# Optimization experiments

Hardware: AMD Instinct MI355X
Metric: run time of the kernel (lower is better)

## Reference

```python
import jax, jax.numpy as jnp
import numpy as np

D_MODEL = 1024
NUM_HEADS = 16
HEAD_DIM = D_MODEL // NUM_HEADS
CAUSAL = True


def rope_cos_sin(seq_len, dim):
    inv_freq = 1.0 / (10000.0 ** (jnp.arange(0, dim, 2, dtype=jnp.float32) / dim))
    t = jnp.arange(seq_len, dtype=jnp.float32)
    freqs = jnp.einsum('i,j->ij', t, inv_freq)          # [S, dim/2]
    emb = jnp.concatenate([freqs, freqs], axis=-1)      # [S, dim]
    return jnp.cos(emb), jnp.sin(emb)


def rotate_half(x):
    x1, x2 = jnp.split(x, 2, axis=-1)
    return jnp.concatenate([-x2, x1], axis=-1)


def setup_inputs() -> dict:
    key = jax.random.key(0)
    k1, k2, k3, k4, k5 = jax.random.split(key, 5)
    B, S = 2, 2048
    x = jax.random.normal(k1, (B, S, D_MODEL), dtype=jnp.float32)
    s = 1.0 / np.sqrt(D_MODEL)
    W_qkv = jax.random.normal(k2, (D_MODEL, 3 * D_MODEL), dtype=jnp.float32) * s
    b_qkv = jax.random.normal(k3, (3 * D_MODEL,), dtype=jnp.float32) * 0.01
    W_out = jax.random.normal(k4, (D_MODEL, D_MODEL), dtype=jnp.float32) * s
    b_out = jax.random.normal(k5, (D_MODEL,), dtype=jnp.float32) * 0.01
    return {"x": x, "W_qkv": W_qkv, "b_qkv": b_qkv, "W_out": W_out, "b_out": b_out}


def reference(x, W_qkv, b_qkv, W_out, b_out):
    B, S, _ = x.shape
    qkv = x @ W_qkv + b_qkv                              # [B, S, 3D]
    q, k, v = jnp.split(qkv, 3, axis=-1)
    # [B, H, S, hd]
    q = q.reshape(B, S, NUM_HEADS, HEAD_DIM).transpose(0, 2, 1, 3)
    k = k.reshape(B, S, NUM_HEADS, HEAD_DIM).transpose(0, 2, 1, 3)
    v = v.reshape(B, S, NUM_HEADS, HEAD_DIM).transpose(0, 2, 1, 3)
    cos, sin = rope_cos_sin(S, HEAD_DIM)                 # [S, hd]
    cos = cos[None, None]
    sin = sin[None, None]
    q = q * cos + rotate_half(q) * sin
    k = k * cos + rotate_half(k) * sin
    scores = jnp.einsum('bhqd,bhkd->bhqk', q, k) / np.sqrt(HEAD_DIM)
    if CAUSAL:
        causal_mask = jnp.triu(jnp.ones((S, S), dtype=bool), k=1)
        scores = jnp.where(causal_mask, -jnp.inf, scores)
    attn = jax.nn.softmax(scores, axis=-1)
    out = jnp.einsum('bhqk,bhkd->bhqd', attn, v)         # [B, H, S, hd]
    out = out.transpose(0, 2, 1, 3).reshape(B, S, D_MODEL)
    return out @ W_out + b_out
```

## Files before the change

### kernel.cpp

```cpp
#include <hip/hip_runtime.h>
#include <hip/hip_bf16.h>
#include <math.h>

typedef __bf16 bf16;
typedef __bf16 bf16x8 __attribute__((ext_vector_type(8)));
typedef unsigned short ushort8 __attribute__((ext_vector_type(8)));
typedef float floatx4 __attribute__((ext_vector_type(4)));

#define MFMA_BF16(a, b, c) __builtin_amdgcn_mfma_f32_16x16x32_bf16(a, b, c, 0, 0, 0)

#define Q_SCALE 0.18033688011112042f
#define NEG_INVFREQ_LOG2 0.41524101186092029f
#define INV_2PI 0.15915494309189535f

#if __has_builtin(__builtin_amdgcn_exp2f)
#define EXP2F(x) __builtin_amdgcn_exp2f(x)
#else
#define EXP2F(x) exp2f(x)
#endif

__device__ __forceinline__ void hw_sincos_rev(float rev, float* sn, float* cs) {
#if __has_builtin(__builtin_amdgcn_sinf) && __has_builtin(__builtin_amdgcn_cosf) && \
    __has_builtin(__builtin_amdgcn_fractf)
  const float f = __builtin_amdgcn_fractf(rev);
  *sn = __builtin_amdgcn_sinf(f);
  *cs = __builtin_amdgcn_cosf(f);
#else
  sincosf(rev * 6.2831853071795864f, sn, cs);
#endif
}

__device__ __forceinline__ bf16x8 cvt8(const float4 a, const float4 b) {
  bf16x8 t;
  t[0] = (bf16)a.x; t[1] = (bf16)a.y; t[2] = (bf16)a.z; t[3] = (bf16)a.w;
  t[4] = (bf16)b.x; t[5] = (bf16)b.y; t[6] = (bf16)b.z; t[7] = (bf16)b.w;
  return t;
}

__device__ __forceinline__ unsigned int pack2(float a, float b) {
#if __has_builtin(__builtin_amdgcn_cvt_pk_bf16_f32)
  return __builtin_bit_cast(unsigned int, __builtin_amdgcn_cvt_pk_bf16_f32(a, b));
#else
  unsigned short lo = __builtin_bit_cast(unsigned short, (bf16)a);
  unsigned short hi = __builtin_bit_cast(unsigned short, (bf16)b);
  return (unsigned int)lo | ((unsigned int)hi << 16);
#endif
}

__device__ __forceinline__ void gld16(const bf16* g, bf16* l) {
  __builtin_amdgcn_global_load_lds(
      (const __attribute__((address_space(1))) unsigned int*)g,
      (__attribute__((address_space(3))) unsigned int*)l, 16, 0, 0);
}

__global__ __launch_bounds__(256) void cast_x_kernel(const float* __restrict__ in,
                                                     bf16* __restrict__ out) {
  const int i = blockIdx.x * 256 + threadIdx.x;
  const float4 a = *(const float4*)&in[(size_t)i * 8];
  const float4 b = *(const float4*)&in[(size_t)i * 8 + 4];
  *(bf16x8*)&out[(size_t)i * 8] = cvt8(a, b);
}

__global__ __launch_bounds__(256) void transpose_w_kernel(
    const float* __restrict__ in, bf16* __restrict__ out, int N, int K) {
  __shared__ __align__(16) bf16 T[64][40];
  const int t = threadIdx.x;
  const int k0 = blockIdx.y * 32, n0 = blockIdx.x * 64;
  {
    const int k = t >> 3, n8 = (t & 7) * 8;
    const float* p = &in[(size_t)(k0 + k) * N + n0 + n8];
    const float4 a = *(const float4*)p;
    const float4 b = *(const float4*)(p + 4);
    const float v[8] = {a.x, a.y, a.z, a.w, b.x, b.y, b.z, b.w};
#pragma unroll
    for (int j = 0; j < 8; j++) {
      const int n = n8 + j;
      T[n][k ^ (8 * ((n >> 3) & 3))] = (bf16)v[j];
    }
  }
  __syncthreads();
  {
    const int n = t >> 2, k8 = (t & 3) * 8;
    const int kp = k8 ^ (8 * ((n >> 3) & 3));
    *(bf16x8*)&out[(size_t)(n0 + n) * K + k0 + k8] = *(const bf16x8*)&T[n][kp];
  }
}

template <int TN, int MODE>
__global__ __launch_bounds__(256) void gemm_kernel(
    const bf16* __restrict__ A, const bf16* __restrict__ Bt,
    const float* __restrict__ bias, void* __restrict__ out0,
    bf16* __restrict__ outK, bf16* __restrict__ outV, int M, int N, int K) {
  constexpr int NI = TN / 32;
  constexpr int BI = TN / 32;
  __shared__ __align__(16) bf16 As2[2][128][32];
  __shared__ __align__(16) bf16 Bs2[2][TN][32];

  const int tid = threadIdx.x, lane = tid & 63, w = tid >> 6;
  const int c = lane & 15, quad = lane >> 4;
  const int wm = w >> 1, wn = w & 1;
  const int m0 = blockIdx.y * 128, n0 = blockIdx.x * TN;
  const int srow = lane >> 2, scol = (lane & 3) * 8;

  floatx4 acc[4][NI] = {};

  for (int k0 = 0; k0 < K; k0 += 64) {
    __syncthreads();
#pragma unroll
    for (int i = 0; i < 4; i++) {
      const int seg = w * 4 + i;
      const int kh = seg >> 3, r0 = (seg & 7) * 16;
      gld16(&A[(size_t)(m0 + r0 + srow) * K + k0 + kh * 32 + scol],
            &As2[kh][r0][0]);
    }
#pragma unroll
    for (int i = 0; i < BI; i++) {
      const int seg = w * BI + i;
      const int kh = seg / (TN / 16), r0 = (seg % (TN / 16)) * 16;
      gld16(&Bt[(size_t)(n0 + r0 + srow) * K + k0 + kh * 32 + scol],
            &Bs2[kh][r0][0]);
    }
    __syncthreads();

#pragma unroll
    for (int kh = 0; kh < 2; kh++) {
      bf16x8 af[4], bfr[NI];
#pragma unroll
      for (int mi = 0; mi < 4; mi++)
        af[mi] = *(const bf16x8*)&As2[kh][wm * 64 + mi * 16 + c][quad * 8];
#pragma unroll
      for (int ni = 0; ni < NI; ni++)
        bfr[ni] = *(const bf16x8*)&Bs2[kh][wn * (TN / 2) + ni * 16 + c][quad * 8];
#pragma unroll
      for (int mi = 0; mi < 4; mi++)
#pragma unroll
        for (int ni = 0; ni < NI; ni++)
          acc[mi][ni] = MFMA_BF16(af[mi], bfr[ni], acc[mi][ni]);
    }
  }

  if (MODE == 0) {
#pragma unroll
    for (int mi = 0; mi < 4; mi++)
#pragma unroll
      for (int ni = 0; ni < NI; ni++)
#pragma unroll
        for (int r = 0; r < 4; r++) {
          const int row = m0 + wm * 64 + mi * 16 + quad * 4 + r;
          const int col = n0 + wn * (TN / 2) + ni * 16 + c;
          ((float*)out0)[(size_t)row * N + col] = acc[mi][ni][r] + bias[col];
        }
  } else {
    const int colb = n0 + wn * (TN / 2);
    const int t = colb >> 10;
    const int h = (colb & 1023) >> 6;
    bf16* dst = (t == 0) ? (bf16*)out0 : (t == 1 ? outK : outV);
    if (t == 2) {
#pragma unroll
      for (int mi = 0; mi < 4; mi++)
#pragma unroll
        for (int ni = 0; ni < NI; ni++)
#pragma unroll
          for (int r = 0; r < 4; r++) {
            const int row = m0 + wm * 64 + mi * 16 + quad * 4 + r;
            const int col = colb + ni * 16 + c;
            const int b = row >> 11, s = row & 2047;
            dst[(((size_t)b * 16 + h) * 2048 + s) * 64 + (col & 63)] =
                (bf16)(acc[mi][ni][r] + bias[col]);
          }
    } else {
      const float qs = (t == 0) ? Q_SCALE : 1.0f;
      const float invr[2] = {exp2f(-NEG_INVFREQ_LOG2 * (float)c) * INV_2PI,
                             exp2f(-NEG_INVFREQ_LOG2 * (float)(16 + c)) * INV_2PI};
#pragma unroll
      for (int mi = 0; mi < 4; mi++) {
#pragma unroll
        for (int r = 0; r < 4; r++) {
          const int row = m0 + wm * 64 + mi * 16 + quad * 4 + r;
          const int b = row >> 11, s = row & 2047;
          const size_t base = (((size_t)b * 16 + h) * 2048 + s) * 64;
#pragma unroll
          for (int ni = 0; ni < 2; ni++) {
            float sn, cs;
            hw_sincos_rev((float)s * invr[ni], &sn, &cs);
            const float v1 = acc[mi][ni][r] + bias[colb + ni * 16 + c];
            const float v2 = acc[mi][ni + 2][r] + bias[colb + (ni + 2) * 16 + c];
            const int d = ni * 16 + c;
            dst[base + d] = (bf16)((v1 * cs - v2 * sn) * qs);
            dst[base + d + 32] = (bf16)((v2 * cs + v1 * sn) * qs);
          }
        }
      }
    }
  }
}

struct AttnState {
  floatx4 o[4];
  float l;
};

__device__ __forceinline__ void attn_step(
    const bf16x8 qf[2], const bf16x8 kf[4][2], const bf16x8 vf[4][2],
    bf16 (*PsW)[72], AttnState& st, int qglob, int kbase, bool diag, int c,
    int quad) {
  floatx4 sacc[4] = {};
#pragma unroll
  for (int kg = 0; kg < 4; kg++)
#pragma unroll
    for (int dh = 0; dh < 2; dh++)
      sacc[kg] = MFMA_BF16(kf[kg][dh], qf[dh], sacc[kg]);

#pragma unroll
  for (int kg = 0; kg < 4; kg++) {
    float p[4];
#pragma unroll
    for (int r = 0; r < 4; r++) {
      float e = EXP2F(sacc[kg][r]);
      if (diag && (kbase + kg * 16 + quad * 4 + r > qglob)) e = 0.0f;
      p[r] = e;
    }
    st.l += (p[0] + p[1]) + (p[2] + p[3]);
    const uint2 u = {pack2(p[0], p[1]), pack2(p[2], p[3])};
    *(uint2*)&PsW[c][kg * 16 + quad * 4] = u;
  }

  bf16x8 pf[2];
#pragma unroll
  for (int ks = 0; ks < 2; ks++)
    pf[ks] = *(const bf16x8*)&PsW[c][ks * 32 + quad * 8];

#pragma unroll
  for (int dg = 0; dg < 4; dg++)
#pragma unroll
    for (int ks = 0; ks < 2; ks++)
      st.o[dg] = MFMA_BF16(vf[dg][ks], pf[ks], st.o[dg]);
}

__global__ __launch_bounds__(256) void attn_kernel(const bf16* __restrict__ Q,
                                                   const bf16* __restrict__ K,
                                                   const bf16* __restrict__ V,
                                                   bf16* __restrict__ Aout) {
  const int S = 2048;
  const int bh = blockIdx.y;
  const int p = blockIdx.x;
  const int tid = threadIdx.x, lane = tid & 63, wave = tid >> 6;
  const int c = lane & 15, quad = lane >> 4;

  __shared__ __align__(16) bf16 Ks2[2][64][32];
  __shared__ __align__(16) bf16 Vt[64][72];
  __shared__ __align__(16) bf16 Ps[4][16][72];

  const bf16* Qb = Q + (size_t)bh * S * 64;
  const bf16* Kb = K + (size_t)bh * S * 64;
  const bf16* Vb = V + (size_t)bh * S * 64;
  const int b = bh >> 4, h = bh & 15;

  const int qA = p, qB = 31 - p;
  const int qgA = qA * 64 + wave * 16 + c;
  const int qgB = qB * 64 + wave * 16 + c;

  bf16x8 qfA[2], qfB[2];
#pragma unroll
  for (int dh = 0; dh < 2; dh++) {
    qfA[dh] = *(const bf16x8*)&Qb[(size_t)qgA * 64 + dh * 32 + quad * 8];
    qfB[dh] = *(const bf16x8*)&Qb[(size_t)qgB * 64 + dh * 32 + quad * 8];
  }

  AttnState stA = {}, stB = {};

  const int vcc = (tid & 7) * 8;
  const int vr2 = ((tid >> 3) + 4 * (tid & 7)) & 31;
  const int ksr = lane >> 2, ksc = (lane & 3) * 8;

  for (int kt = 0; kt <= qB; kt++) {
    __syncthreads();
#pragma unroll
    for (int i = 0; i < 2; i++) {
      const int seg = wave * 2 + i;
      const int dh = seg >> 2, r0 = (seg & 3) * 16;
      gld16(&Kb[(size_t)(kt * 64 + r0 + ksr) * 64 + dh * 32 + ksc],
            &Ks2[dh][r0][0]);
    }
    {
      const bf16* vs = &Vb[(size_t)(kt * 64 + 2 * vr2) * 64 + vcc];
      const ushort8 w0 = __builtin_bit_cast(ushort8, *(const bf16x8*)vs);
      const ushort8 w1 = __builtin_bit_cast(ushort8, *(const bf16x8*)(vs + 64));
#pragma unroll
      for (int j = 0; j < 8; j++)
        *(unsigned int*)&Vt[vcc + j][2 * vr2] =
            (unsigned int)w0[j] | ((unsigned int)w1[j] << 16);
    }
    __syncthreads();

    bf16x8 kf[4][2];
#pragma unroll
    for (int kg = 0; kg < 4; kg++)
#pragma unroll
      for (int dh = 0; dh < 2; dh++)
        kf[kg][dh] = *(const bf16x8*)&Ks2[dh][kg * 16 + c][quad * 8];

    bf16x8 vf[4][2];
#pragma unroll
    for (int dg = 0; dg < 4; dg++)
#pragma unroll
      for (int ks = 0; ks < 2; ks++)
        vf[dg][ks] = *(const bf16x8*)&Vt[dg * 16 + c][ks * 32 + quad * 8];

    attn_step(qfB, kf, vf, Ps[wave], stB, qgB, kt * 64, kt == qB, c, quad);
    if (kt <= qA)
      attn_step(qfA, kf, vf, Ps[wave], stA, qgA, kt * 64, kt == qA, c, quad);
  }

  stA.l += __shfl_xor(stA.l, 16);
  stA.l += __shfl_xor(stA.l, 32);
  stB.l += __shfl_xor(stB.l, 16);
  stB.l += __shfl_xor(stB.l, 32);
  const float ivA = 1.0f / stA.l, ivB = 1.0f / stB.l;

#pragma unroll
  for (int dg = 0; dg < 4; dg++) {
    const uint2 uA = {pack2(stA.o[dg][0] * ivA, stA.o[dg][1] * ivA),
                      pack2(stA.o[dg][2] * ivA, stA.o[dg][3] * ivA)};
    const uint2 uB = {pack2(stB.o[dg][0] * ivB, stB.o[dg][1] * ivB),
                      pack2(stB.o[dg][2] * ivB, stB.o[dg][3] * ivB)};
    *(uint2*)&Aout[((size_t)b * 2048 + qgA) * 1024 + h * 64 + dg * 16 + quad * 4] = uA;
    *(uint2*)&Aout[((size_t)b * 2048 + qgB) * 1024 + h * 64 + dg * 16 + quad * 4] = uB;
  }
}

extern "C" void kernel_launch(void* const* d_in, const int* in_sizes, int n_in,
                              void* d_out, int out_size, void* d_ws,
                              size_t ws_size, hipStream_t stream) {
  const float* x = (const float*)d_in[0];
  const float* W_qkv = (const float*)d_in[1];
  const float* b_qkv = (const float*)d_in[2];
  const float* W_out = (const float*)d_in[3];
  const float* b_out = (const float*)d_in[4];
  float* out = (float*)d_out;

  const int B = 2, S = 2048, NH = 16;
  const size_t qn = (size_t)B * NH * S * 64;

  bf16* xb = (bf16*)d_ws;
  bf16* Wqkvt = xb + qn;
  bf16* Wot = Wqkvt + 3072 * 1024;
  bf16* Qw = Wot + 1024 * 1024;
  bf16* Kw = Qw + qn;
  bf16* Vw = Kw + qn;
  bf16* AO = xb;

  cast_x_kernel<<<dim3(qn / 8 / 256), 256, 0, stream>>>(x, xb);
  transpose_w_kernel<<<dim3(3072 / 64, 1024 / 32), 256, 0, stream>>>(
      W_qkv, Wqkvt, 3072, 1024);
  transpose_w_kernel<<<dim3(1024 / 64, 1024 / 32), 256, 0, stream>>>(
      W_out, Wot, 1024, 1024);

  gemm_kernel<128, 1><<<dim3(3072 / 128, 4096 / 128), 256, 0, stream>>>(
      xb, Wqkvt, b_qkv, Qw, Kw, Vw, 4096, 3072, 1024);
  attn_kernel<<<dim3(16, B * NH), 256, 0, stream>>>(Qw, Kw, Vw, AO);
  gemm_kernel<64, 0><<<dim3(1024 / 64, 4096 / 128), 256, 0, stream>>>(
      AO, Wot, b_out, out, nullptr, nullptr, 4096, 1024, 1024);
}
```

Before: 199.2 us.

## Double-buffer K and V tiles in LDS to prefetch next tile during compute

Splits the K and transposed-V shared-memory tiles into two buffers. While the current tile is used for QK^T and PV, the next K tile is issued via direct global-to-LDS loads and the next V tile is loaded into registers, then written transposed to LDS after compute. The loop drops from two barriers per iteration to one, aiming to hide global memory latency. In exchange it doubles LDS use for K/V and holds the prefetched V values in registers across the compute, which may reduce occupancy.

After: 192.7 us. 3.3% less time.

```diff
diff --git a/kernel.cpp b/kernel.cpp
--- a/kernel.cpp
+++ b/kernel.cpp
@@ -247,8 +247,8 @@
   const int tid = threadIdx.x, lane = tid & 63, wave = tid >> 6;
   const int c = lane & 15, quad = lane >> 4;
 
-  __shared__ __align__(16) bf16 Ks2[2][64][32];
-  __shared__ __align__(16) bf16 Vt[64][72];
+  __shared__ __align__(16) bf16 Ks2[2][2][64][32];
+  __shared__ __align__(16) bf16 Vt[2][64][72];
   __shared__ __align__(16) bf16 Ps[4][16][72];
 
   const bf16* Qb = Q + (size_t)bh * S * 64;
@@ -273,43 +273,66 @@
   const int vr2 = ((tid >> 3) + 4 * (tid & 7)) & 31;
   const int ksr = lane >> 2, ksc = (lane & 3) * 8;
 
-  for (int kt = 0; kt <= qB; kt++) {
-    __syncthreads();
+  {
 #pragma unroll
     for (int i = 0; i < 2; i++) {
       const int seg = wave * 2 + i;
       const int dh = seg >> 2, r0 = (seg & 3) * 16;
-      gld16(&Kb[(size_t)(kt * 64 + r0 + ksr) * 64 + dh * 32 + ksc],
-            &Ks2[dh][r0][0]);
-    }
-    {
-      const bf16* vs = &Vb[(size_t)(kt * 64 + 2 * vr2) * 64 + vcc];
-      const ushort8 w0 = __builtin_bit_cast(ushort8, *(const bf16x8*)vs);
-      const ushort8 w1 = __builtin_bit_cast(ushort8, *(const bf16x8*)(vs + 64));
-#pragma unroll
-      for (int j = 0; j < 8; j++)
-        *(unsigned int*)&Vt[vcc + j][2 * vr2] =
-            (unsigned int)w0[j] | ((unsigned int)w1[j] << 16);
-    }
-    __syncthreads();
+      gld16(&Kb[(size_t)(r0 + ksr) * 64 + dh * 32 + ksc], &Ks2[0][dh][r0][0]);
+    }
+    const bf16* vs = &Vb[(size_t)(2 * vr2) * 64 + vcc];
+    const ushort8 w0 = __builtin_bit_cast(ushort8, *(const bf16x8*)vs);
+    const ushort8 w1 = __builtin_bit_cast(ushort8, *(const bf16x8*)(vs + 64));
+#pragma unroll
+    for (int j = 0; j < 8; j++)
+      *(unsigned int*)&Vt[0][vcc + j][2 * vr2] =
+          (unsigned int)w0[j] | ((unsigned int)w1[j] << 16);
+  }
+  __syncthreads();
+
+  int buf = 0;
+  for (int kt = 0; kt <= qB; kt++) {
+    const bool pfetch = (kt < qB);
+    ushort8 nw0, nw1;
+    if (pfetch) {
+      const bf16* vs = &Vb[(size_t)((kt + 1) * 64 + 2 * vr2) * 64 + vcc];
+      nw0 = __builtin_bit_cast(ushort8, *(const bf16x8*)vs);
+      nw1 = __builtin_bit_cast(ushort8, *(const bf16x8*)(vs + 64));
+#pragma unroll
+      for (int i = 0; i < 2; i++) {
+        const int seg = wave * 2 + i;
+        const int dh = seg >> 2, r0 = (seg & 3) * 16;
+        gld16(&Kb[(size_t)((kt + 1) * 64 + r0 + ksr) * 64 + dh * 32 + ksc],
+              &Ks2[buf ^ 1][dh][r0][0]);
+      }
+    }
 
     bf16x8 kf[4][2];
 #pragma unroll
     for (int kg = 0; kg < 4; kg++)
 #pragma unroll
       for (int dh = 0; dh < 2; dh++)
-        kf[kg][dh] = *(const bf16x8*)&Ks2[dh][kg * 16 + c][quad * 8];
+        kf[kg][dh] = *(const bf16x8*)&Ks2[buf][dh][kg * 16 + c][quad * 8];
 
     bf16x8 vf[4][2];
 #pragma unroll
     for (int dg = 0; dg < 4; dg++)
 #pragma unroll
       for (int ks = 0; ks < 2; ks++)
-        vf[dg][ks] = *(const bf16x8*)&Vt[dg * 16 + c][ks * 32 + quad * 8];
+        vf[dg][ks] = *(const bf16x8*)&Vt[buf][dg * 16 + c][ks * 32 + quad * 8];
 
     attn_step(qfB, kf, vf, Ps[wave], stB, qgB, kt * 64, kt == qB, c, quad);
     if (kt <= qA)
       attn_step(qfA, kf, vf, Ps[wave], stA, qgA, kt * 64, kt == qA, c, quad);
+
+    if (pfetch) {
+#pragma unroll
+      for (int j = 0; j < 8; j++)
+        *(unsigned int*)&Vt[buf ^ 1][vcc + j][2 * vr2] =
+            (unsigned int)nw0[j] | ((unsigned int)nw1[j] << 16);
+    }
+    __syncthreads();
+    buf ^= 1;
   }
 
   stA.l += __shfl_xor(stA.l, 16);
```
